# Optimization experiments

Hardware: AMD Instinct MI355X
Metric: run time of the kernel (lower is better)

## Reference

```python
import jax, jax.numpy as jnp
import numpy as np

N_NODES = 10000
N_EDGES = 320000
N_GRAPHS = 16


def _sage_layer(h, src, dst, W_self, W_neigh, b):
    # DGL SAGEConv('mean'): out_i = h_i @ W_self + mean_{j in N_in(i)} h_j @ W_neigh + b
    msg_sum = jax.ops.segment_sum(h[src], dst, num_segments=N_NODES)
    deg = jax.ops.segment_sum(jnp.ones(src.shape[0], h.dtype), dst, num_segments=N_NODES)
    h_neigh = msg_sum / jnp.maximum(deg, 1.0)[:, None]
    return h @ W_self + h_neigh @ W_neigh + b


def _segment_mean(x, seg, num_segments):
    s = jax.ops.segment_sum(x, seg, num_segments=num_segments)
    c = jax.ops.segment_sum(jnp.ones(x.shape[0], x.dtype), seg, num_segments=num_segments)
    return s / jnp.maximum(c, 1.0)[:, None]


def setup_inputs() -> dict:
    key = jax.random.key(0)
    ks = jax.random.split(key, 16)
    d_in, d_h, n_cls = 256, 64, 2

    def glorot(k, shape):
        fan_in = shape[0]
        return jax.random.normal(k, shape, dtype=jnp.float32) / np.sqrt(fan_in)

    return {
        "feat": jax.random.normal(ks[0], (N_NODES, d_in), dtype=jnp.float32),
        "src": jax.random.randint(ks[1], (N_EDGES,), 0, N_NODES),
        "dst": jax.random.randint(ks[2], (N_EDGES,), 0, N_NODES),
        "graph_id": jnp.sort(jax.random.randint(ks[3], (N_NODES,), 0, N_GRAPHS)),
        "W_self1": glorot(ks[4], (d_in, d_h)),
        "W_neigh1": glorot(ks[5], (d_in, d_h)),
        "b1": jnp.zeros((d_h,), jnp.float32),
        "W_self2": glorot(ks[6], (d_h, d_h)),
        "W_neigh2": glorot(ks[7], (d_h, d_h)),
        "b2": jnp.zeros((d_h,), jnp.float32),
        "W_self3": glorot(ks[8], (d_h, d_h)),
        "W_neigh3": glorot(ks[9], (d_h, d_h)),
        "b3": jnp.zeros((d_h,), jnp.float32),
        "W_cls": glorot(ks[10], (d_h, n_cls)),
        "b_cls": jnp.zeros((n_cls,), jnp.float32),
    }


def reference(feat, src, dst, graph_id, W_self1, W_neigh1, b1, W_self2, W_neigh2, b2,
              W_self3, W_neigh3, b3, W_cls, b_cls):
    # layer 1 + relu (dropout is identity in eval mode)
    h = jax.nn.relu(_sage_layer(feat, src, dst, W_self1, W_neigh1, b1))
    # layer 2 + relu
    h = jax.nn.relu(_sage_layer(h, src, dst, W_self2, W_neigh2, b2))
    # layer 3 (no activation)
    h = _sage_layer(h, src, dst, W_self3, W_neigh3, b3)
    # dgl.mean_nodes readout per graph
    out_feat = _segment_mean(h, graph_id, N_GRAPHS)
    out = out_feat @ W_cls + b_cls
    return (out, out_feat, h)
```

## Files before the change

kernel.cpp:

```cpp
#include <hip/hip_runtime.h>


#define DH 64
#define NG 16
#define NSB 8
#define DTILES 32
#define MAXNPB 1250
#define CAP 32

__device__ __forceinline__ unsigned short f2bf(float f) {
    unsigned int u = __float_as_uint(f);
    unsigned int r = (u + 0x7FFFu + ((u >> 16) & 1u)) >> 16;
    return (unsigned short)r;
}
__device__ __forceinline__ float bfu(unsigned short v) {
    return __uint_as_float(((unsigned int)v) << 16);
}
__device__ __forceinline__ int deg8(const int* __restrict__ cnt8, int n) {
    const int4* cp = reinterpret_cast<const int4*>(&cnt8[n * NSB]);
    int4 c0 = cp[0], c1 = cp[1];
    return c0.x + c0.y + c0.z + c0.w + c1.x + c1.y + c1.z + c1.w;
}

__global__ void build_kernel(const int* __restrict__ src, const int* __restrict__ dst,
                             int* __restrict__ cnt8, int* __restrict__ es,
                             int E, int npb8) {
    int i = blockIdx.x * blockDim.x + threadIdx.x;
    if (i < E) {
        int s = src[i];
        int k = dst[i] * NSB + s / npb8;
        int p = atomicAdd(&cnt8[k], 1);
        if (p < CAP) es[(size_t)k * CAP + p] = s;
    }
}

template <int K, bool FUSE>
__global__ __launch_bounds__(256) void gemm_dual_kernel(
    const float* __restrict__ X, const float* __restrict__ Ws_g,
    const float* __restrict__ Wn_g, const float* __restrict__ bias,
    const float* __restrict__ Hn_in, const int* __restrict__ cnt8,
    float* __restrict__ S, unsigned short* __restrict__ P,
    float* __restrict__ Hn_out, int M) {
    __shared__ float Xs[64][68];
    __shared__ float Ws[64][68];
    __shared__ float Wn[64][68];
    int tid = threadIdx.x;
    int row0 = blockIdx.x * 64;
    int cx = tid & 15;
    int ry = tid >> 4;
    float acc_s[4][4] = {{0.f}};
    float acc_n[4][4] = {{0.f}};

    for (int kc = 0; kc < K; kc += 64) {
#pragma unroll
        for (int it = 0; it < 4; ++it) {
            int q = tid + 256 * it;
            int row = q >> 4;
            int k4 = (q & 15) * 4;
            float4 xv = make_float4(0.f, 0.f, 0.f, 0.f);
            int gr = row0 + row;
            if (gr < M) {
                xv = *reinterpret_cast<const float4*>(&X[(size_t)gr * K + kc + k4]);
                if constexpr (FUSE) {
                    float4 hv = *reinterpret_cast<const float4*>(&Hn_in[(size_t)gr * DH + k4]);
                    float inv = 1.f / fmaxf((float)deg8(cnt8, gr), 1.f);
                    xv.x = fmaxf(fmaf(hv.x, inv, xv.x), 0.f);
                    xv.y = fmaxf(fmaf(hv.y, inv, xv.y), 0.f);
                    xv.z = fmaxf(fmaf(hv.z, inv, xv.z), 0.f);
                    xv.w = fmaxf(fmaf(hv.w, inv, xv.w), 0.f);
                }
            }
            *reinterpret_cast<float4*>(&Xs[row][k4]) = xv;
            float4 wv = *reinterpret_cast<const float4*>(&Ws_g[(size_t)(kc + row) * 64 + k4]);
            *reinterpret_cast<float4*>(&Ws[row][k4]) = wv;
            float4 nv = *reinterpret_cast<const float4*>(&Wn_g[(size_t)(kc + row) * 64 + k4]);
            *reinterpret_cast<float4*>(&Wn[row][k4]) = nv;
        }
        __syncthreads();
#pragma unroll 4
        for (int kk = 0; kk < 64; ++kk) {
            float a[4], bs[4], bn[4];
#pragma unroll
            for (int j = 0; j < 4; ++j) a[j] = Xs[ry * 4 + j][kk];
#pragma unroll
            for (int i = 0; i < 4; ++i) {
                bs[i] = Ws[kk][cx + 16 * i];
                bn[i] = Wn[kk][cx + 16 * i];
            }
#pragma unroll
            for (int j = 0; j < 4; ++j)
#pragma unroll
                for (int i = 0; i < 4; ++i) {
                    acc_s[j][i] += a[j] * bs[i];
                    acc_n[j][i] += a[j] * bn[i];
                }
        }
        __syncthreads();
    }

#pragma unroll
    for (int j = 0; j < 4; ++j) {
        int r = row0 + ry * 4 + j;
        if (r < M) {
#pragma unroll
            for (int i = 0; i < 4; ++i) {
                int col = cx + 16 * i;
                S[(size_t)r * DH + col] = acc_s[j][i] + bias[col];
                P[(size_t)r * DH + col] = f2bf(acc_n[j][i]);
                Hn_out[(size_t)r * DH + col] = 0.f;
            }
        }
    }
}

__global__ __launch_bounds__(1024) void agg_kernel(
    const unsigned short* __restrict__ P, const int* __restrict__ cnt8,
    const int* __restrict__ es, float* __restrict__ Hn, int M, int npb8) {
    __shared__ __align__(16) unsigned short sP[MAXNPB * DH];
    int tid = threadIdx.x;
    int sb    = blockIdx.x & (NSB - 1);
    int dtile = blockIdx.x >> 3;
    int s0 = sb * npb8;
    int snodes = min(npb8, M - s0);

    {
        const uint4* gp = reinterpret_cast<const uint4*>(P + (size_t)s0 * DH);
        int cnt = snodes * 8;
        for (int j = tid; j < cnt; j += 1024)
            *reinterpret_cast<uint4*>(&sP[j * 8]) = gp[j];
    }
    __syncthreads();

    int lane = tid & 63, wid = tid >> 6;
    int dpb  = (M + DTILES - 1) / DTILES;
    int d0t  = dtile * dpb;
    int dend = min(d0t + dpb, M);

    for (int dst = d0t + wid; dst < dend; dst += 16) {
        int key = dst * NSB + sb;
        int cnt = min(cnt8[key], CAP);
        if (cnt == 0) continue;
        size_t base = (size_t)key * CAP;
        float acc = 0.f;
        int cmax = cnt - 1;
        for (int e = 0; e < cnt; e += 4) {
            int i0 = es[base + min(e + 0, cmax)] - s0;
            int i1 = es[base + min(e + 1, cmax)] - s0;
            int i2 = es[base + min(e + 2, cmax)] - s0;
            int i3 = es[base + min(e + 3, cmax)] - s0;
            float m1 = (e + 1 < cnt) ? 1.f : 0.f;
            float m2 = (e + 2 < cnt) ? 1.f : 0.f;
            float m3 = (e + 3 < cnt) ? 1.f : 0.f;
            float f0 = bfu(sP[(size_t)i0 * DH + lane]);
            float f1 = bfu(sP[(size_t)i1 * DH + lane]);
            float f2 = bfu(sP[(size_t)i2 * DH + lane]);
            float f3 = bfu(sP[(size_t)i3 * DH + lane]);
            acc += f0;
            acc = fmaf(m1, f1, acc);
            acc = fmaf(m2, f2, acc);
            acc = fmaf(m3, f3, acc);
        }
        atomicAdd(&Hn[(size_t)dst * DH + lane], acc);
    }
}

__global__ __launch_bounds__(256) void finish_kernel(
    const float* __restrict__ S, const float* __restrict__ Hn,
    const int* __restrict__ cnt8, const int* __restrict__ graph_id,
    float* __restrict__ H, float* __restrict__ gsum, float* __restrict__ gcnt,
    int M) {
    int lane = threadIdx.x & 63;
    int wid  = blockIdx.x * 4 + (threadIdx.x >> 6);
    int nw   = gridDim.x * 4;
    int cpw  = (M + nw - 1) / nw;
    int n0 = wid * cpw, n1 = min(n0 + cpw, M);
    if (n0 >= n1) return;

    float acc = 0.f;
    int cnt = 0;
    int cur = graph_id[n0];
    for (int n = n0; n < n1; ++n) {
        int gid = graph_id[n];
        if (gid != cur) {
            atomicAdd(&gsum[cur * DH + lane], acc);
            if (lane == 0) atomicAdd(&gcnt[cur], (float)cnt);
            acc = 0.f; cnt = 0; cur = gid;
        }
        float inv = 1.f / fmaxf((float)deg8(cnt8, n), 1.f);
        size_t o = (size_t)n * DH + lane;
        float val = fmaf(Hn[o], inv, S[o]);
        H[o] = val;
        acc += val;
        ++cnt;
    }
    atomicAdd(&gsum[cur * DH + lane], acc);
    if (lane == 0) atomicAdd(&gcnt[cur], (float)cnt);
}

__global__ __launch_bounds__(1024) void readout_kernel(
    const float* __restrict__ gsum, const float* __restrict__ gcnt,
    const float* __restrict__ Wc, const float* __restrict__ bc,
    float* __restrict__ out, float* __restrict__ out_feat) {
    __shared__ float ofs[NG][DH];
    int tid = threadIdx.x;
    int g = tid >> 6, d = tid & 63;
    float of = gsum[tid] / fmaxf(gcnt[g], 1.0f);
    out_feat[tid] = of;
    ofs[g][d] = of;
    __syncthreads();
    if (tid < NG * 2) {
        int gg = tid >> 1, cc = tid & 1;
        float acc = bc[cc];
#pragma unroll 8
        for (int dd = 0; dd < DH; ++dd) acc += ofs[gg][dd] * Wc[dd * 2 + cc];
        out[gg * 2 + cc] = acc;
    }
}

extern "C" void kernel_launch(void* const* d_in, const int* in_sizes, int n_in,
                              void* d_out, int out_size, void* d_ws, size_t ws_size,
                              hipStream_t stream) {
    const float* feat     = (const float*)d_in[0];
    const int*   src      = (const int*)d_in[1];
    const int*   dst      = (const int*)d_in[2];
    const int*   graph_id = (const int*)d_in[3];
    const float* Ws1 = (const float*)d_in[4];
    const float* Wn1 = (const float*)d_in[5];
    const float* b1  = (const float*)d_in[6];
    const float* Ws2 = (const float*)d_in[7];
    const float* Wn2 = (const float*)d_in[8];
    const float* b2  = (const float*)d_in[9];
    const float* Ws3 = (const float*)d_in[10];
    const float* Wn3 = (const float*)d_in[11];
    const float* b3  = (const float*)d_in[12];
    const float* Wc  = (const float*)d_in[13];
    const float* bc  = (const float*)d_in[14];

    const int M  = in_sizes[3];
    const int E  = in_sizes[1];
    const int M2 = M * NSB;
    const int npb8 = (M + NSB - 1) / NSB;

    float* out      = (float*)d_out;
    float* out_feat = out + NG * 2;
    float* Hbuf     = out_feat + NG * DH;

    char* w = (char*)d_ws;
    size_t off = 0;
    auto carve = [&](size_t bytes) {
        size_t o = off;
        off = (off + bytes + 255) & ~(size_t)255;
        return o;
    };
    int*   cnt8  = (int*)  (w + carve((size_t)M2 * 4));
    float* gsum  = (float*)(w + carve((size_t)NG * DH * 4));
    float* gcnt  = (float*)(w + carve((size_t)NG * 4));
    size_t zero_bytes = off;
    int*   es    = (int*)  (w + carve((size_t)M2 * CAP * 4));
    float* Sbuf  = (float*)(w + carve((size_t)M * DH * 4));
    unsigned short* Pbuf = (unsigned short*)(w + carve((size_t)M * DH * 2));
    float* Hn    = (float*)(w + carve((size_t)M * DH * 4));
    (void)ws_size; (void)n_in; (void)out_size;

    (void)hipMemsetAsync(d_ws, 0, zero_bytes, stream);

    int eb = (E + 255) / 256;
    build_kernel<<<eb, 256, 0, stream>>>(src, dst, cnt8, es, E, npb8);

    int gb = (M + 63) / 64;
    int ab = NSB * DTILES;
    int fb = 160;

    gemm_dual_kernel<256, false><<<gb, 256, 0, stream>>>(
        feat, Ws1, Wn1, b1, nullptr, nullptr, Sbuf, Pbuf, Hn, M);
    agg_kernel<<<ab, 1024, 0, stream>>>(Pbuf, cnt8, es, Hn, M, npb8);

    gemm_dual_kernel<64, true><<<gb, 256, 0, stream>>>(
        Sbuf, Ws2, Wn2, b2, Hn, cnt8, Sbuf, Pbuf, Hn, M);
    agg_kernel<<<ab, 1024, 0, stream>>>(Pbuf, cnt8, es, Hn, M, npb8);

    gemm_dual_kernel<64, true><<<gb, 256, 0, stream>>>(
        Sbuf, Ws3, Wn3, b3, Hn, cnt8, Sbuf, Pbuf, Hn, M);
    agg_kernel<<<ab, 1024, 0, stream>>>(Pbuf, cnt8, es, Hn, M, npb8);

    finish_kernel<<<fb, 256, 0, stream>>>(Sbuf, Hn, cnt8, graph_id,
                                          Hbuf, gsum, gcnt, M);
    readout_kernel<<<1, 1024, 0, stream>>>(gsum, gcnt, Wc, bc, out, out_feat);
}
```

Baseline: 255.9 us.

## Fuse all GNN layers into a persistent megakernel with software grid barriers

Replaces the eight separate launches (build, three GEMM/aggregate pairs, finish, readout) with one persistent kernel of 256 blocks of 1024 threads that synchronizes phases through an atomic grid barrier. It also changes the source-bucketing from 8 to 16 shards, halving per-block LDS staging. The goal is to remove launch gaps and tail effects between small kernels. In exchange, only a quarter of threads do the GEMM work, the barrier relies on all blocks being co-resident, and build and GEMM1 run with no barrier between them.

```diff
diff --git a/kernel.cpp b/kernel.cpp
--- a/kernel.cpp
+++ b/kernel.cpp
@@ -3,10 +3,13 @@
 
 #define DH 64
 #define NG 16
-#define NSB 8
-#define DTILES 32
-#define MAXNPB 1250
+#define NSB 16
+#define DTILES 16
+#define MAXNPB 625
 #define CAP 32
+#define MEGA_BLOCKS 256
+#define MEGA_THREADS 1024
+#define NW_FIN 640
 
 __device__ __forceinline__ unsigned short f2bf(float f) {
     unsigned int u = __float_as_uint(f);
@@ -16,138 +19,170 @@
 __device__ __forceinline__ float bfu(unsigned short v) {
     return __uint_as_float(((unsigned int)v) << 16);
 }
-__device__ __forceinline__ int deg8(const int* __restrict__ cnt8, int n) {
-    const int4* cp = reinterpret_cast<const int4*>(&cnt8[n * NSB]);
-    int4 c0 = cp[0], c1 = cp[1];
-    return c0.x + c0.y + c0.z + c0.w + c1.x + c1.y + c1.z + c1.w;
-}
-
-__global__ void build_kernel(const int* __restrict__ src, const int* __restrict__ dst,
-                             int* __restrict__ cnt8, int* __restrict__ es,
-                             int E, int npb8) {
-    int i = blockIdx.x * blockDim.x + threadIdx.x;
-    if (i < E) {
-        int s = src[i];
-        int k = dst[i] * NSB + s / npb8;
-        int p = atomicAdd(&cnt8[k], 1);
-        if (p < CAP) es[(size_t)k * CAP + p] = s;
+__device__ __forceinline__ int degN(const int* __restrict__ cnt, int n) {
+    const int4* cp = reinterpret_cast<const int4*>(&cnt[n * NSB]);
+    int4 c0 = cp[0], c1 = cp[1], c2 = cp[2], c3 = cp[3];
+    return c0.x + c0.y + c0.z + c0.w + c1.x + c1.y + c1.z + c1.w +
+           c2.x + c2.y + c2.z + c2.w + c3.x + c3.y + c3.z + c3.w;
+}
+
+struct MegaArgs {
+    const float* feat; const int* src; const int* dst; const int* graph_id;
+    const float* Ws1; const float* Wn1; const float* b1;
+    const float* Ws2; const float* Wn2; const float* b2;
+    const float* Ws3; const float* Wn3; const float* b3;
+    const float* Wc; const float* bc;
+    int* cnt16; int* es; int* bar;
+    float* S; unsigned short* P; float* Hn;
+    float* out; float* out_feat; float* H;
+    float* gsum; float* gcnt;
+    int M, E, npb;
+};
+
+__device__ __forceinline__ void grid_sync(int* cnt, int* gen, int nb) {
+    __syncthreads();
+    if (threadIdx.x == 0) {
+        __threadfence();
+        int g = __hip_atomic_load(gen, __ATOMIC_RELAXED, __HIP_MEMORY_SCOPE_AGENT);
+        int a = __hip_atomic_fetch_add(cnt, 1, __ATOMIC_ACQ_REL, __HIP_MEMORY_SCOPE_AGENT);
+        if (a == nb - 1) {
+            __hip_atomic_store(cnt, 0, __ATOMIC_RELAXED, __HIP_MEMORY_SCOPE_AGENT);
+            __hip_atomic_fetch_add(gen, 1, __ATOMIC_RELEASE, __HIP_MEMORY_SCOPE_AGENT);
+        } else {
+            while (__hip_atomic_load(gen, __ATOMIC_ACQUIRE, __HIP_MEMORY_SCOPE_AGENT) == g)
+                __builtin_amdgcn_s_sleep(2);
+        }
+        __threadfence();
+    }
+    __syncthreads();
+}
+
+__device__ __forceinline__ void build_phase(const MegaArgs& a) {
+    int idx = blockIdx.x * MEGA_THREADS + threadIdx.x;
+    int stride = gridDim.x * MEGA_THREADS;
+    for (int i = idx; i < a.E; i += stride) {
+        int s = a.src[i];
+        int k = a.dst[i] * NSB + s / a.npb;
+        int p = atomicAdd(&a.cnt16[k], 1);
+        if (p < CAP) a.es[(size_t)k * CAP + p] = s;
     }
 }
 
 template <int K, bool FUSE>
-__global__ __launch_bounds__(256) void gemm_dual_kernel(
-    const float* __restrict__ X, const float* __restrict__ Ws_g,
-    const float* __restrict__ Wn_g, const float* __restrict__ bias,
-    const float* __restrict__ Hn_in, const int* __restrict__ cnt8,
-    float* __restrict__ S, unsigned short* __restrict__ P,
-    float* __restrict__ Hn_out, int M) {
-    __shared__ float Xs[64][68];
-    __shared__ float Ws[64][68];
-    __shared__ float Wn[64][68];
-    int tid = threadIdx.x;
-    int row0 = blockIdx.x * 64;
-    int cx = tid & 15;
-    int ry = tid >> 4;
-    float acc_s[4][4] = {{0.f}};
-    float acc_n[4][4] = {{0.f}};
-
-    for (int kc = 0; kc < K; kc += 64) {
-#pragma unroll
-        for (int it = 0; it < 4; ++it) {
-            int q = tid + 256 * it;
-            int row = q >> 4;
-            int k4 = (q & 15) * 4;
-            float4 xv = make_float4(0.f, 0.f, 0.f, 0.f);
-            int gr = row0 + row;
-            if (gr < M) {
-                xv = *reinterpret_cast<const float4*>(&X[(size_t)gr * K + kc + k4]);
-                if constexpr (FUSE) {
-                    float4 hv = *reinterpret_cast<const float4*>(&Hn_in[(size_t)gr * DH + k4]);
-                    float inv = 1.f / fmaxf((float)deg8(cnt8, gr), 1.f);
-                    xv.x = fmaxf(fmaf(hv.x, inv, xv.x), 0.f);
-                    xv.y = fmaxf(fmaf(hv.y, inv, xv.y), 0.f);
-                    xv.z = fmaxf(fmaf(hv.z, inv, xv.z), 0.f);
-                    xv.w = fmaxf(fmaf(hv.w, inv, xv.w), 0.f);
+__device__ void gemm_phase(const MegaArgs& a, const float* __restrict__ X,
+                           const float* __restrict__ Ws_g,
+                           const float* __restrict__ Wn_g,
+                           const float* __restrict__ bias, char* smem) {
+    float (*Xs)[68] = reinterpret_cast<float (*)[68]>(smem);
+    float (*Ws)[68] = reinterpret_cast<float (*)[68]>(smem + 17408);
+    float (*Wn)[68] = reinterpret_cast<float (*)[68]>(smem + 34816);
+    const int tid = threadIdx.x;
+    const int cx = tid & 15;
+    const int ry = (tid >> 4) & 15;
+    const int ntiles = (a.M + 63) >> 6;
+
+    for (int tile = blockIdx.x; tile < ntiles; tile += gridDim.x) {
+        const int row0 = tile * 64;
+        float acc_s[4][4] = {{0.f}};
+        float acc_n[4][4] = {{0.f}};
+
+        for (int kc = 0; kc < K; kc += 64) {
+            {
+                int row = tid >> 4;
+                int k4  = (tid & 15) * 4;
+                int gr = row0 + row;
+                float4 xv = make_float4(0.f, 0.f, 0.f, 0.f);
+                if (gr < a.M) {
+                    xv = *reinterpret_cast<const float4*>(&X[(size_t)gr * K + kc + k4]);
+                    if constexpr (FUSE) {
+                        float4 hv = *reinterpret_cast<const float4*>(&a.Hn[(size_t)gr * DH + k4]);
+                        float inv = 1.f / fmaxf((float)degN(a.cnt16, gr), 1.f);
+                        xv.x = fmaxf(fmaf(hv.x, inv, xv.x), 0.f);
+                        xv.y = fmaxf(fmaf(hv.y, inv, xv.y), 0.f);
+                        xv.z = fmaxf(fmaf(hv.z, inv, xv.z), 0.f);
+                        xv.w = fmaxf(fmaf(hv.w, inv, xv.w), 0.f);
+                    }
+                }
+                *reinterpret_cast<float4*>(&Xs[row][k4]) = xv;
+                *reinterpret_cast<float4*>(&Ws[row][k4]) =
+                    *reinterpret_cast<const float4*>(&Ws_g[(size_t)(kc + row) * 64 + k4]);
+                *reinterpret_cast<float4*>(&Wn[row][k4]) =
+                    *reinterpret_cast<const float4*>(&Wn_g[(size_t)(kc + row) * 64 + k4]);
+            }
+            __syncthreads();
+            if (tid < 256) {
+#pragma unroll 4
+                for (int kk = 0; kk < 64; ++kk) {
+                    float av[4], bs[4], bn[4];
+#pragma unroll
+                    for (int j = 0; j < 4; ++j) av[j] = Xs[ry * 4 + j][kk];
+#pragma unroll
+                    for (int i = 0; i < 4; ++i) {
+                        bs[i] = Ws[kk][cx + 16 * i];
+                        bn[i] = Wn[kk][cx + 16 * i];
+                    }
+#pragma unroll
+                    for (int j = 0; j < 4; ++j)
+#pragma unroll
+                        for (int i = 0; i < 4; ++i) {
+                            acc_s[j][i] += av[j] * bs[i];
+                            acc_n[j][i] += av[j] * bn[i];
+                        }
                 }
             }
-            *reinterpret_cast<float4*>(&Xs[row][k4]) = xv;
-            float4 wv = *reinterpret_cast<const float4*>(&Ws_g[(size_t)(kc + row) * 64 + k4]);
-            *reinterpret_cast<float4*>(&Ws[row][k4]) = wv;
-            float4 nv = *reinterpret_cast<const float4*>(&Wn_g[(size_t)(kc + row) * 64 + k4]);
-            *reinterpret_cast<float4*>(&Wn[row][k4]) = nv;
-        }
-        __syncthreads();
-#pragma unroll 4
-        for (int kk = 0; kk < 64; ++kk) {
-            float a[4], bs[4], bn[4];
-#pragma unroll
-            for (int j = 0; j < 4; ++j) a[j] = Xs[ry * 4 + j][kk];
-#pragma unroll
-            for (int i = 0; i < 4; ++i) {
-                bs[i] = Ws[kk][cx + 16 * i];
-                bn[i] = Wn[kk][cx + 16 * i];
+            __syncthreads();
+        }
+        if (tid < 256) {
+#pragma unroll
+            for (int j = 0; j < 4; ++j) {
+                int r = row0 + ry * 4 + j;
+                if (r < a.M) {
+#pragma unroll
+                    for (int i = 0; i < 4; ++i) {
+                        int col = cx + 16 * i;
+                        a.S[(size_t)r * DH + col] = acc_s[j][i] + bias[col];
+                        a.P[(size_t)r * DH + col] = f2bf(acc_n[j][i]);
+                        a.Hn[(size_t)r * DH + col] = 0.f;
+                    }
+                }
             }
-#pragma unroll
-            for (int j = 0; j < 4; ++j)
-#pragma unroll
-                for (int i = 0; i < 4; ++i) {
-                    acc_s[j][i] += a[j] * bs[i];
-                    acc_n[j][i] += a[j] * bn[i];
-                }
-        }
-        __syncthreads();
-    }
-
-#pragma unroll
-    for (int j = 0; j < 4; ++j) {
-        int r = row0 + ry * 4 + j;
-        if (r < M) {
-#pragma unroll
-            for (int i = 0; i < 4; ++i) {
-                int col = cx + 16 * i;
-                S[(size_t)r * DH + col] = acc_s[j][i] + bias[col];
-                P[(size_t)r * DH + col] = f2bf(acc_n[j][i]);
-                Hn_out[(size_t)r * DH + col] = 0.f;
-            }
-        }
-    }
-}
-
-__global__ __launch_bounds__(1024) void agg_kernel(
-    const unsigned short* __restrict__ P, const int* __restrict__ cnt8,
-    const int* __restrict__ es, float* __restrict__ Hn, int M, int npb8) {
-    __shared__ __align__(16) unsigned short sP[MAXNPB * DH];
-    int tid = threadIdx.x;
-    int sb    = blockIdx.x & (NSB - 1);
-    int dtile = blockIdx.x >> 3;
-    int s0 = sb * npb8;
-    int snodes = min(npb8, M - s0);
+        }
+    }
+}
+
+__device__ void agg_phase(const MegaArgs& a, char* smem) {
+    unsigned short* sP = reinterpret_cast<unsigned short*>(smem);
+    const int tid = threadIdx.x;
+    const int sb    = blockIdx.x & (NSB - 1);
+    const int dtile = blockIdx.x >> 4;
+    const int s0 = sb * a.npb;
+    const int snodes = min(a.npb, a.M - s0);
 
     {
-        const uint4* gp = reinterpret_cast<const uint4*>(P + (size_t)s0 * DH);
+        const uint4* gp = reinterpret_cast<const uint4*>(a.P + (size_t)s0 * DH);
         int cnt = snodes * 8;
-        for (int j = tid; j < cnt; j += 1024)
+        for (int j = tid; j < cnt; j += MEGA_THREADS)
             *reinterpret_cast<uint4*>(&sP[j * 8]) = gp[j];
     }
     __syncthreads();
 
-    int lane = tid & 63, wid = tid >> 6;
-    int dpb  = (M + DTILES - 1) / DTILES;
+    const int lane = tid & 63, wv = tid >> 6;
+    int dpb  = (a.M + DTILES - 1) / DTILES;
     int d0t  = dtile * dpb;
-    int dend = min(d0t + dpb, M);
-
-    for (int dst = d0t + wid; dst < dend; dst += 16) {
-        int key = dst * NSB + sb;
-        int cnt = min(cnt8[key], CAP);
+    int dend = min(d0t + dpb, a.M);
+
+    for (int dstn = d0t + wv; dstn < dend; dstn += 16) {
+        int key = dstn * NSB + sb;
+        int cnt = min(a.cnt16[key], CAP);
         if (cnt == 0) continue;
         size_t base = (size_t)key * CAP;
         float acc = 0.f;
         int cmax = cnt - 1;
         for (int e = 0; e < cnt; e += 4) {
-            int i0 = es[base + min(e + 0, cmax)] - s0;
-            int i1 = es[base + min(e + 1, cmax)] - s0;
-            int i2 = es[base + min(e + 2, cmax)] - s0;
-            int i3 = es[base + min(e + 3, cmax)] - s0;
+            int i0 = a.es[base + min(e + 0, cmax)] - s0;
+            int i1 = a.es[base + min(e + 1, cmax)] - s0;
+            int i2 = a.es[base + min(e + 2, cmax)] - s0;
+            int i3 = a.es[base + min(e + 3, cmax)] - s0;
             float m1 = (e + 1 < cnt) ? 1.f : 0.f;
             float m2 = (e + 2 < cnt) ? 1.f : 0.f;
             float m3 = (e + 3 < cnt) ? 1.f : 0.f;
@@ -160,61 +195,81 @@
             acc = fmaf(m2, f2, acc);
             acc = fmaf(m3, f3, acc);
         }
-        atomicAdd(&Hn[(size_t)dst * DH + lane], acc);
-    }
-}
-
-__global__ __launch_bounds__(256) void finish_kernel(
-    const float* __restrict__ S, const float* __restrict__ Hn,
-    const int* __restrict__ cnt8, const int* __restrict__ graph_id,
-    float* __restrict__ H, float* __restrict__ gsum, float* __restrict__ gcnt,
-    int M) {
-    int lane = threadIdx.x & 63;
-    int wid  = blockIdx.x * 4 + (threadIdx.x >> 6);
-    int nw   = gridDim.x * 4;
-    int cpw  = (M + nw - 1) / nw;
-    int n0 = wid * cpw, n1 = min(n0 + cpw, M);
+        atomicAdd(&a.Hn[(size_t)dstn * DH + lane], acc);
+    }
+    __syncthreads();
+}
+
+__device__ void finish_phase(const MegaArgs& a) {
+    const int lane = threadIdx.x & 63;
+    const int wv = threadIdx.x >> 6;
+    int wid = blockIdx.x + MEGA_BLOCKS * wv;
+    if (wid >= NW_FIN) return;
+    int cpw = (a.M + NW_FIN - 1) / NW_FIN;
+    int n0 = wid * cpw, n1 = min(n0 + cpw, a.M);
     if (n0 >= n1) return;
 
     float acc = 0.f;
     int cnt = 0;
-    int cur = graph_id[n0];
+    int cur = a.graph_id[n0];
     for (int n = n0; n < n1; ++n) {
-        int gid = graph_id[n];
+        int gid = a.graph_id[n];
         if (gid != cur) {
-            atomicAdd(&gsum[cur * DH + lane], acc);
-            if (lane == 0) atomicAdd(&gcnt[cur], (float)cnt);
+            atomicAdd(&a.gsum[cur * DH + lane], acc);
+            if (lane == 0) atomicAdd(&a.gcnt[cur], (float)cnt);
             acc = 0.f; cnt = 0; cur = gid;
         }
-        float inv = 1.f / fmaxf((float)deg8(cnt8, n), 1.f);
+        float inv = 1.f / fmaxf((float)degN(a.cnt16, n), 1.f);
         size_t o = (size_t)n * DH + lane;
-        float val = fmaf(Hn[o], inv, S[o]);
-        H[o] = val;
+        float val = fmaf(a.Hn[o], inv, a.S[o]);
+        a.H[o] = val;
         acc += val;
         ++cnt;
     }
-    atomicAdd(&gsum[cur * DH + lane], acc);
-    if (lane == 0) atomicAdd(&gcnt[cur], (float)cnt);
-}
-
-__global__ __launch_bounds__(1024) void readout_kernel(
-    const float* __restrict__ gsum, const float* __restrict__ gcnt,
-    const float* __restrict__ Wc, const float* __restrict__ bc,
-    float* __restrict__ out, float* __restrict__ out_feat) {
-    __shared__ float ofs[NG][DH];
+    atomicAdd(&a.gsum[cur * DH + lane], acc);
+    if (lane == 0) atomicAdd(&a.gcnt[cur], (float)cnt);
+}
+
+__device__ void readout_phase(const MegaArgs& a, char* smem) {
+    if (blockIdx.x != 0) return;
+    float (*ofs)[DH] = reinterpret_cast<float (*)[DH]>(smem);
     int tid = threadIdx.x;
     int g = tid >> 6, d = tid & 63;
-    float of = gsum[tid] / fmaxf(gcnt[g], 1.0f);
-    out_feat[tid] = of;
+    float of = a.gsum[tid] / fmaxf(a.gcnt[g], 1.0f);
+    a.out_feat[tid] = of;
     ofs[g][d] = of;
     __syncthreads();
     if (tid < NG * 2) {
         int gg = tid >> 1, cc = tid & 1;
-        float acc = bc[cc];
+        float accv = a.bc[cc];
 #pragma unroll 8
-        for (int dd = 0; dd < DH; ++dd) acc += ofs[gg][dd] * Wc[dd * 2 + cc];
-        out[gg * 2 + cc] = acc;
-    }
+        for (int dd = 0; dd < DH; ++dd) accv += ofs[gg][dd] * a.Wc[dd * 2 + cc];
+        a.out[gg * 2 + cc] = accv;
+    }
+}
+
+__global__ __launch_bounds__(MEGA_THREADS, 8) void mega_kernel(MegaArgs a) {
+    __shared__ __align__(16) char smem[80000];
+    int* bcnt = a.bar;
+    int* bgen = a.bar + 1;
+    const int nb = gridDim.x;
+
+    build_phase(a);
+    gemm_phase<256, false>(a, a.feat, a.Ws1, a.Wn1, a.b1, smem);
+    grid_sync(bcnt, bgen, nb);
+    agg_phase(a, smem);
+    grid_sync(bcnt, bgen, nb);
+    gemm_phase<64, true>(a, a.S, a.Ws2, a.Wn2, a.b2, smem);
+    grid_sync(bcnt, bgen, nb);
+    agg_phase(a, smem);
+    grid_sync(bcnt, bgen, nb);
+    gemm_phase<64, true>(a, a.S, a.Ws3, a.Wn3, a.b3, smem);
+    grid_sync(bcnt, bgen, nb);
+    agg_phase(a, smem);
+    grid_sync(bcnt, bgen, nb);
+    finish_phase(a);
+    grid_sync(bcnt, bgen, nb);
+    readout_phase(a, smem);
 }
 
 extern "C" void kernel_launch(void* const* d_in, const int* in_sizes, int n_in,
@@ -239,7 +294,7 @@
     const int M  = in_sizes[3];
     const int E  = in_sizes[1];
     const int M2 = M * NSB;
-    const int npb8 = (M + NSB - 1) / NSB;
+    const int npb = (M + NSB - 1) / NSB;
 
     float* out      = (float*)d_out;
     float* out_feat = out + NG * 2;
@@ -252,9 +307,10 @@
         off = (off + bytes + 255) & ~(size_t)255;
         return o;
     };
-    int*   cnt8  = (int*)  (w + carve((size_t)M2 * 4));
+    int*   cnt16 = (int*)  (w + carve((size_t)M2 * 4));
     float* gsum  = (float*)(w + carve((size_t)NG * DH * 4));
     float* gcnt  = (float*)(w + carve((size_t)NG * 4));
+    int*   bar   = (int*)  (w + carve(2 * 4));
     size_t zero_bytes = off;
     int*   es    = (int*)  (w + carve((size_t)M2 * CAP * 4));
     float* Sbuf  = (float*)(w + carve((size_t)M * DH * 4));
@@ -264,26 +320,17 @@
 
     (void)hipMemsetAsync(d_ws, 0, zero_bytes, stream);
 
-    int eb = (E + 255) / 256;
-    build_kernel<<<eb, 256, 0, stream>>>(src, dst, cnt8, es, E, npb8);
-
-    int gb = (M + 63) / 64;
-    int ab = NSB * DTILES;
-    int fb = 160;
-
-    gemm_dual_kernel<256, false><<<gb, 256, 0, stream>>>(
-        feat, Ws1, Wn1, b1, nullptr, nullptr, Sbuf, Pbuf, Hn, M);
-    agg_kernel<<<ab, 1024, 0, stream>>>(Pbuf, cnt8, es, Hn, M, npb8);
-
-    gemm_dual_kernel<64, true><<<gb, 256, 0, stream>>>(
-        Sbuf, Ws2, Wn2, b2, Hn, cnt8, Sbuf, Pbuf, Hn, M);
-    agg_kernel<<<ab, 1024, 0, stream>>>(Pbuf, cnt8, es, Hn, M, npb8);
-
-    gemm_dual_kernel<64, true><<<gb, 256, 0, stream>>>(
-        Sbuf, Ws3, Wn3, b3, Hn, cnt8, Sbuf, Pbuf, Hn, M);
-    agg_kernel<<<ab, 1024, 0, stream>>>(Pbuf, cnt8, es, Hn, M, npb8);
-
-    finish_kernel<<<fb, 256, 0, stream>>>(Sbuf, Hn, cnt8, graph_id,
-                                          Hbuf, gsum, gcnt, M);
-    readout_kernel<<<1, 1024, 0, stream>>>(gsum, gcnt, Wc, bc, out, out_feat);
-}
+    MegaArgs a;
+    a.feat = feat; a.src = src; a.dst = dst; a.graph_id = graph_id;
+    a.Ws1 = Ws1; a.Wn1 = Wn1; a.b1 = b1;
+    a.Ws2 = Ws2; a.Wn2 = Wn2; a.b2 = b2;
+    a.Ws3 = Ws3; a.Wn3 = Wn3; a.b3 = b3;
+    a.Wc = Wc; a.bc = bc;
+    a.cnt16 = cnt16; a.es = es; a.bar = bar;
+    a.S = Sbuf; a.P = Pbuf; a.Hn = Hn;
+    a.out = out; a.out_feat = out_feat; a.H = Hbuf;
+    a.gsum = gsum; a.gcnt = gcnt;
+    a.M = M; a.E = E; a.npb = npb;
+
+    mega_kernel<<<MEGA_BLOCKS, MEGA_THREADS, 0, stream>>>(a);
+}
```

Result: slower. 876.2 us (+242.5%).
